# Optimization experiments

Measured on AMD Instinct MI355X. Metric: run time of the kernel, lower is better.

Reference implementation:

```python
import jax, jax.numpy as jnp
import numpy as np

B, T, H = 32, 2048, 1024

def setup_inputs() -> dict:
    key = jax.random.key(0)
    ks = jax.random.split(key, 9)
    s = 1.0 / np.sqrt(H)
    return {
        "encoder_outputs": jax.random.normal(ks[0], (B, T, H), jnp.float32),
        "decoder_output": jax.random.normal(ks[1], (1, B, H), jnp.float32),
        "Wk": jax.random.uniform(ks[2], (H, H), jnp.float32, -s, s),
        "bk": jax.random.uniform(ks[3], (H,), jnp.float32, -s, s),
        "Wq": jax.random.uniform(ks[4], (H, H), jnp.float32, -s, s),
        "bq": jax.random.uniform(ks[5], (H,), jnp.float32, -s, s),
        "Wout": jax.random.uniform(ks[6], (H,), jnp.float32, -s, s),
        "bout": jax.random.uniform(ks[7], (), jnp.float32, -s, s),
        "inputs": jax.random.randint(ks[8], (B, T), 0, 32000, jnp.int32),  # unused, as in original
    }

def reference(encoder_outputs, decoder_output, Wk, bk, Wq, bq, Wout, bout, inputs):
    # decoder_output: [1, B, H] -> [B, 1, H]
    dec = jnp.swapaxes(decoder_output, 0, 1)
    k = encoder_outputs @ Wk.T + bk          # [B, T, H]
    q = dec @ Wq.T + bq                      # [B, 1, H]
    score = jnp.tanh(k + q) @ Wout + bout    # [B, T]  (linear_out squeezed)
    attn = jax.nn.softmax(score, axis=-1)    # [B, T]
    context = jnp.einsum('bt,bth->bh', attn, encoder_outputs)  # [B, H]
    return context[:, None, :]               # [B, 1, H]
```

## Files before the change

### kernel.cpp

```cpp
#include <hip/hip_runtime.h>
#include <cmath>
#include <stdint.h>

#define B_ 32
#define T_ 2048
#define H_ 1024

typedef __attribute__((ext_vector_type(8))) __bf16 bf16x8;
typedef __attribute__((ext_vector_type(4))) float f32x4;

__device__ inline void async_copy16(const void* g, void* l) {
    __builtin_amdgcn_global_load_lds((const __attribute__((address_space(1))) uint32_t*)g,
                                     (__attribute__((address_space(3))) uint32_t*)l, 16, 0, 0);
}

__device__ inline float fast_tanh(float x) {
    float e = __expf(2.f * x);
    return 1.f - 2.f / (e + 1.f);
}

__global__ __launch_bounds__(256) void zero_kernel(float* __restrict__ p, int n) {
    int i = blockIdx.x * 256 + threadIdx.x;
    if (i < n) p[i] = 0.f;
}

__global__ __launch_bounds__(256) void convert_kernel(const float* __restrict__ in,
                                                      __bf16* __restrict__ out) {
    size_t i = (size_t)(blockIdx.x * 256 + threadIdx.x) * 8;
    const float4* p = (const float4*)(in + i);
    float4 v0 = p[0], v1 = p[1];
    bf16x8 o;
    o[0] = (__bf16)v0.x; o[1] = (__bf16)v0.y; o[2] = (__bf16)v0.z; o[3] = (__bf16)v0.w;
    o[4] = (__bf16)v1.x; o[5] = (__bf16)v1.y; o[6] = (__bf16)v1.z; o[7] = (__bf16)v1.w;
    *(bf16x8*)(out + i) = o;
}

__global__ __launch_bounds__(256) void q_kernel(const float* __restrict__ dec,
                                                const float* __restrict__ Wq,
                                                const float* __restrict__ bq,
                                                const float* __restrict__ bk,
                                                float* __restrict__ kq) {
    int b = blockIdx.x;
    int hc = blockIdx.y;
    __shared__ float ds[H_];
    for (int i = threadIdx.x; i < H_; i += 256) ds[i] = dec[b * H_ + i];
    __syncthreads();
    int h = hc * 256 + threadIdx.x;
    const float4* w = (const float4*)(Wq + (size_t)h * H_);
    float acc = 0.f;
#pragma unroll 8
    for (int j = 0; j < H_ / 4; j++) {
        float4 v = w[j];
        acc += v.x * ds[4 * j] + v.y * ds[4 * j + 1] + v.z * ds[4 * j + 2] + v.w * ds[4 * j + 3];
    }
    kq[b * H_ + h] = acc + bq[h] + bk[h];
}

__global__ __launch_bounds__(256) void score_mfma(const __bf16* __restrict__ encb,
                                                  const __bf16* __restrict__ Wkb,
                                                  const float* __restrict__ kq,
                                                  const float* __restrict__ Wout,
                                                  float* __restrict__ score) {
    __shared__ __align__(16) __bf16 As[512 * 8];
    __shared__ __align__(16) __bf16 Bs[512 * 8];

    const int h0 = blockIdx.x * 128;
    const int m0 = blockIdx.y * 128;
    const int b = m0 >> 11;
    const int tid = threadIdx.x;
    const int lane = tid & 63;
    const int w = tid >> 6;
    const int wm = w & 1, wn = w >> 1;
    const int q4 = lane >> 4, l15 = lane & 15;

    const int S0 = w * 128 + lane;
    const int S1 = S0 + 64;
    const int kg0 = S0 >> 7, row0 = S0 & 127;
    const int kg1 = S1 >> 7, row1 = S1 & 127;
    const __bf16* gA0 = encb + (size_t)(m0 + row0) * H_ + kg0 * 8;
    const __bf16* gA1 = encb + (size_t)(m0 + row1) * H_ + kg1 * 8;
    const __bf16* gB0 = Wkb + (size_t)(h0 + row0) * H_ + kg0 * 8;
    const __bf16* gB1 = Wkb + (size_t)(h0 + row1) * H_ + kg1 * 8;
    __bf16* lA0 = As + (size_t)(w * 128) * 8;
    __bf16* lA1 = As + (size_t)(w * 128 + 64) * 8;
    __bf16* lB0 = Bs + (size_t)(w * 128) * 8;
    __bf16* lB1 = Bs + (size_t)(w * 128 + 64) * 8;

    f32x4 acc[4][4];
#pragma unroll
    for (int i = 0; i < 4; i++)
#pragma unroll
        for (int j = 0; j < 4; j++) acc[i][j] = (f32x4){0.f, 0.f, 0.f, 0.f};

    for (int k0 = 0; k0 < H_; k0 += 32) {
        __syncthreads();
        async_copy16(gA0 + k0, lA0);
        async_copy16(gA1 + k0, lA1);
        async_copy16(gB0 + k0, lB0);
        async_copy16(gB1 + k0, lB1);
        __syncthreads();

        bf16x8 a[4], bb[4];
#pragma unroll
        for (int mf = 0; mf < 4; mf++)
            a[mf] = *(const bf16x8*)(As + (size_t)(q4 * 128 + wm * 64 + mf * 16 + l15) * 8);
#pragma unroll
        for (int nf = 0; nf < 4; nf++)
            bb[nf] = *(const bf16x8*)(Bs + (size_t)(q4 * 128 + wn * 64 + nf * 16 + l15) * 8);
#pragma unroll
        for (int mf = 0; mf < 4; mf++)
#pragma unroll
            for (int nf = 0; nf < 4; nf++)
                acc[mf][nf] = __builtin_amdgcn_mfma_f32_16x16x32_bf16(a[mf], bb[nf], acc[mf][nf], 0, 0, 0);
    }

    float wv[4], kqv[4];
#pragma unroll
    for (int nf = 0; nf < 4; nf++) {
        int h = h0 + wn * 64 + nf * 16 + l15;
        wv[nf] = Wout[h];
        kqv[nf] = kq[b * H_ + h];
    }
#pragma unroll
    for (int mf = 0; mf < 4; mf++) {
#pragma unroll
        for (int r = 0; r < 4; r++) {
            float s = 0.f;
#pragma unroll
            for (int nf = 0; nf < 4; nf++)
                s += wv[nf] * fast_tanh(acc[mf][nf][r] + kqv[nf]);
#pragma unroll
            for (int m = 1; m < 16; m <<= 1) s += __shfl_xor(s, m, 64);
            if (l15 == 0)
                atomicAdd(&score[m0 + wm * 64 + mf * 16 + q4 * 4 + r], s);
        }
    }
}

#define BK 32
#define ASTR 68
#define BSTR 132
__global__ __launch_bounds__(256) void score_fp32(const float* __restrict__ enc,
                                                  const float* __restrict__ Wk,
                                                  const float* __restrict__ kq,
                                                  const float* __restrict__ Wout,
                                                  float* __restrict__ score) {
    __shared__ __align__(16) float As[BK * ASTR];
    __shared__ __align__(16) float Bs[BK * BSTR];
    __shared__ float wout_s[128];
    __shared__ float kq_s[128];
    const int m0 = blockIdx.x * 64;
    const int h0 = blockIdx.y * 128;
    const int b = m0 >> 11;
    const int tid = threadIdx.x;
    const int tx = tid & 15;
    const int ty = tid >> 4;
    if (tid < 128) {
        wout_s[tid] = Wout[h0 + tid];
        kq_s[tid] = kq[b * H_ + h0 + tid];
    }
    float acc[4][8];
#pragma unroll
    for (int i = 0; i < 4; i++)
#pragma unroll
        for (int j = 0; j < 8; j++) acc[i][j] = 0.f;
    for (int k0 = 0; k0 < H_; k0 += BK) {
        __syncthreads();
#pragma unroll
        for (int r = 0; r < 2; r++) {
            int li = tid + r * 256;
            int tok = li >> 3, kg = li & 7;
            float4 v = *(const float4*)(enc + (size_t)(m0 + tok) * H_ + k0 + kg * 4);
            As[(kg * 4 + 0) * ASTR + tok] = v.x;
            As[(kg * 4 + 1) * ASTR + tok] = v.y;
            As[(kg * 4 + 2) * ASTR + tok] = v.z;
            As[(kg * 4 + 3) * ASTR + tok] = v.w;
        }
#pragma unroll
        for (int r = 0; r < 4; r++) {
            int li = tid + r * 256;
            int h = li >> 3, kg = li & 7;
            float4 v = *(const float4*)(Wk + (size_t)(h0 + h) * H_ + k0 + kg * 4);
            Bs[(kg * 4 + 0) * BSTR + h] = v.x;
            Bs[(kg * 4 + 1) * BSTR + h] = v.y;
            Bs[(kg * 4 + 2) * BSTR + h] = v.z;
            Bs[(kg * 4 + 3) * BSTR + h] = v.w;
        }
        __syncthreads();
#pragma unroll
        for (int kk = 0; kk < BK; kk++) {
            float4 a4 = *(const float4*)&As[kk * ASTR + ty * 4];
            float4 b4a = *(const float4*)&Bs[kk * BSTR + tx * 4];
            float4 b4b = *(const float4*)&Bs[kk * BSTR + 64 + tx * 4];
            float av[4] = {a4.x, a4.y, a4.z, a4.w};
            float bv[8] = {b4a.x, b4a.y, b4a.z, b4a.w, b4b.x, b4b.y, b4b.z, b4b.w};
#pragma unroll
            for (int i = 0; i < 4; i++)
#pragma unroll
                for (int j = 0; j < 8; j++) acc[i][j] += av[i] * bv[j];
        }
    }
    float wv[8], kqv[8];
#pragma unroll
    for (int j = 0; j < 8; j++) {
        int hl = (j < 4) ? (tx * 4 + j) : (64 + tx * 4 + (j - 4));
        wv[j] = wout_s[hl];
        kqv[j] = kq_s[hl];
    }
#pragma unroll
    for (int i = 0; i < 4; i++) {
        float s = 0.f;
#pragma unroll
        for (int j = 0; j < 8; j++) s += wv[j] * tanhf(acc[i][j] + kqv[j]);
#pragma unroll
        for (int m = 1; m < 16; m <<= 1) s += __shfl_xor(s, m, 64);
        if (tx == 0) atomicAdd(&score[m0 + ty * 4 + i], s);
    }
}

__global__ __launch_bounds__(256) void softmax_kernel(float* __restrict__ score) {
    int b = blockIdx.x, tid = threadIdx.x;
    float* s = score + b * T_;
    __shared__ float red[8];
    float v[8];
    float mx = -1e30f;
#pragma unroll
    for (int i = 0; i < 8; i++) {
        v[i] = s[tid + i * 256];
        mx = fmaxf(mx, v[i]);
    }
#pragma unroll
    for (int m = 32; m >= 1; m >>= 1) mx = fmaxf(mx, __shfl_xor(mx, m, 64));
    if ((tid & 63) == 0) red[tid >> 6] = mx;
    __syncthreads();
    mx = fmaxf(fmaxf(red[0], red[1]), fmaxf(red[2], red[3]));
    float sum = 0.f;
#pragma unroll
    for (int i = 0; i < 8; i++) {
        v[i] = __expf(v[i] - mx);
        sum += v[i];
    }
#pragma unroll
    for (int m = 32; m >= 1; m >>= 1) sum += __shfl_xor(sum, m, 64);
    if ((tid & 63) == 0) red[4 + (tid >> 6)] = sum;
    __syncthreads();
    sum = red[4] + red[5] + red[6] + red[7];
    float inv = 1.f / sum;
#pragma unroll
    for (int i = 0; i < 8; i++) s[tid + i * 256] = v[i] * inv;
}

__global__ __launch_bounds__(256) void context_kernel(const float* __restrict__ enc,
                                                      const float* __restrict__ attn,
                                                      float* __restrict__ out) {
    int ts = blockIdx.x, b = blockIdx.y;
    const float* e = enc + (size_t)b * T_ * H_ + (size_t)ts * 64 * H_ + threadIdx.x * 4;
    const float* a = attn + b * T_ + ts * 64;
    float4 acc = {0.f, 0.f, 0.f, 0.f};
#pragma unroll 4
    for (int t = 0; t < 64; t++) {
        float av = a[t];
        float4 v = *(const float4*)(e + (size_t)t * H_);
        acc.x += av * v.x; acc.y += av * v.y; acc.z += av * v.z; acc.w += av * v.w;
    }
    float* o = out + b * H_ + threadIdx.x * 4;
    atomicAdd(o + 0, acc.x);
    atomicAdd(o + 1, acc.y);
    atomicAdd(o + 2, acc.z);
    atomicAdd(o + 3, acc.w);
}

extern "C" void kernel_launch(void* const* d_in, const int* in_sizes, int n_in,
                              void* d_out, int out_size, void* d_ws, size_t ws_size,
                              hipStream_t stream) {
    const float* enc = (const float*)d_in[0];
    const float* dec = (const float*)d_in[1];
    const float* Wk = (const float*)d_in[2];
    const float* bk = (const float*)d_in[3];
    const float* Wq = (const float*)d_in[4];
    const float* bq = (const float*)d_in[5];
    const float* Wout = (const float*)d_in[6];
    float* out = (float*)d_out;

    const size_t encb_bytes = (size_t)B_ * T_ * H_ * 2;
    const size_t wkb_bytes = (size_t)H_ * H_ * 2;
    const size_t need = encb_bytes + wkb_bytes + (size_t)B_ * H_ * 4 + (size_t)B_ * T_ * 4;

    if (ws_size >= need) {
        __bf16* encb = (__bf16*)d_ws;
        __bf16* Wkb = (__bf16*)((char*)d_ws + encb_bytes);
        float* kq = (float*)((char*)d_ws + encb_bytes + wkb_bytes);
        float* score = kq + B_ * H_;

        convert_kernel<<<(B_ * T_ * H_) / 2048, 256, 0, stream>>>(enc, encb);
        convert_kernel<<<(H_ * H_) / 2048, 256, 0, stream>>>(Wk, Wkb);
        q_kernel<<<dim3(B_, 4), 256, 0, stream>>>(dec, Wq, bq, bk, kq);
        zero_kernel<<<(B_ * T_ + 255) / 256, 256, 0, stream>>>(score, B_ * T_);
        zero_kernel<<<(B_ * H_ + 255) / 256, 256, 0, stream>>>(out, B_ * H_);
        score_mfma<<<dim3(8, 512), 256, 0, stream>>>(encb, Wkb, kq, Wout, score);
        softmax_kernel<<<B_, 256, 0, stream>>>(score);
        context_kernel<<<dim3(32, B_), 256, 0, stream>>>(enc, score, out);
    } else {
        float* kq = (float*)d_ws;
        float* score = kq + B_ * H_;
        q_kernel<<<dim3(B_, 4), 256, 0, stream>>>(dec, Wq, bq, bk, kq);
        zero_kernel<<<(B_ * T_ + 255) / 256, 256, 0, stream>>>(score, B_ * T_);
        zero_kernel<<<(B_ * H_ + 255) / 256, 256, 0, stream>>>(out, B_ * H_);
        score_fp32<<<dim3(1024, 8), 256, 0, stream>>>(enc, Wk, kq, Wout, score);
        softmax_kernel<<<B_, 256, 0, stream>>>(score);
        context_kernel<<<dim3(32, B_), 256, 0, stream>>>(enc, score, out);
    }
}
```

Before: 761.2 us.

## Deepen MFMA K-tile, remap blocks per XCD, replace atomics with partial-sum buffers

The score GEMM now stages a 64-wide K slice per iteration instead of 32, halving barrier and loop overhead. It also uses a 1D grid whose block index is remapped so that M-tiles sharing the same XCD reuse L2. Atomic score accumulation is replaced by 16 per-column-slice partial buffers that the softmax kernel sums. The context atomics are likewise replaced by per-chunk partials plus a separate reduce kernel, which drops the zero kernels. The cost is more workspace, extra global traffic for the partials, one more launch, and larger shared memory per block that may lower occupancy.

```diff
diff --git a/kernel.cpp b/kernel.cpp
--- a/kernel.cpp
+++ b/kernel.cpp
@@ -60,12 +60,16 @@
                                                   const __bf16* __restrict__ Wkb,
                                                   const float* __restrict__ kq,
                                                   const float* __restrict__ Wout,
-                                                  float* __restrict__ score) {
-    __shared__ __align__(16) __bf16 As[512 * 8];
-    __shared__ __align__(16) __bf16 Bs[512 * 8];
-
-    const int h0 = blockIdx.x * 128;
-    const int m0 = blockIdx.y * 128;
+                                                  float* __restrict__ sp) {
+    __shared__ __align__(16) __bf16 As[1024 * 8];
+    __shared__ __align__(16) __bf16 Bs[1024 * 8];
+
+    const int bid = blockIdx.x;
+    const int xcd = bid & 7;
+    const int g = (bid >> 3) & 7;
+    const int mt = (bid >> 6) * 8 + xcd;
+    const int h0 = g * 128;
+    const int m0 = mt * 128;
     const int b = m0 >> 11;
     const int tid = threadIdx.x;
     const int lane = tid & 63;
@@ -73,18 +77,19 @@
     const int wm = w & 1, wn = w >> 1;
     const int q4 = lane >> 4, l15 = lane & 15;
 
-    const int S0 = w * 128 + lane;
-    const int S1 = S0 + 64;
-    const int kg0 = S0 >> 7, row0 = S0 & 127;
-    const int kg1 = S1 >> 7, row1 = S1 & 127;
-    const __bf16* gA0 = encb + (size_t)(m0 + row0) * H_ + kg0 * 8;
-    const __bf16* gA1 = encb + (size_t)(m0 + row1) * H_ + kg1 * 8;
-    const __bf16* gB0 = Wkb + (size_t)(h0 + row0) * H_ + kg0 * 8;
-    const __bf16* gB1 = Wkb + (size_t)(h0 + row1) * H_ + kg1 * 8;
-    __bf16* lA0 = As + (size_t)(w * 128) * 8;
-    __bf16* lA1 = As + (size_t)(w * 128 + 64) * 8;
-    __bf16* lB0 = Bs + (size_t)(w * 128) * 8;
-    __bf16* lB1 = Bs + (size_t)(w * 128 + 64) * 8;
+    int kgs[4], rows[4];
+    const __bf16 *gA[4], *gB[4];
+    __bf16 *lA[4], *lB[4];
+#pragma unroll
+    for (int r = 0; r < 4; r++) {
+        int S = w * 256 + r * 64 + lane;
+        kgs[r] = S >> 7;
+        rows[r] = S & 127;
+        gA[r] = encb + (size_t)(m0 + rows[r]) * H_ + kgs[r] * 8;
+        gB[r] = Wkb + (size_t)(h0 + rows[r]) * H_ + kgs[r] * 8;
+        lA[r] = As + (size_t)(w * 256 + r * 64) * 8;
+        lB[r] = Bs + (size_t)(w * 256 + r * 64) * 8;
+    }
 
     f32x4 acc[4][4];
 #pragma unroll
@@ -92,26 +97,29 @@
 #pragma unroll
         for (int j = 0; j < 4; j++) acc[i][j] = (f32x4){0.f, 0.f, 0.f, 0.f};
 
-    for (int k0 = 0; k0 < H_; k0 += 32) {
+    for (int k0 = 0; k0 < H_; k0 += 64) {
         __syncthreads();
-        async_copy16(gA0 + k0, lA0);
-        async_copy16(gA1 + k0, lA1);
-        async_copy16(gB0 + k0, lB0);
-        async_copy16(gB1 + k0, lB1);
+#pragma unroll
+        for (int r = 0; r < 4; r++) async_copy16(gA[r] + k0, lA[r]);
+#pragma unroll
+        for (int r = 0; r < 4; r++) async_copy16(gB[r] + k0, lB[r]);
         __syncthreads();
 
-        bf16x8 a[4], bb[4];
-#pragma unroll
-        for (int mf = 0; mf < 4; mf++)
-            a[mf] = *(const bf16x8*)(As + (size_t)(q4 * 128 + wm * 64 + mf * 16 + l15) * 8);
-#pragma unroll
-        for (int nf = 0; nf < 4; nf++)
-            bb[nf] = *(const bf16x8*)(Bs + (size_t)(q4 * 128 + wn * 64 + nf * 16 + l15) * 8);
-#pragma unroll
-        for (int mf = 0; mf < 4; mf++)
+#pragma unroll
+        for (int kb = 0; kb < 2; kb++) {
+            bf16x8 a[4], bb[4];
+#pragma unroll
+            for (int mf = 0; mf < 4; mf++)
+                a[mf] = *(const bf16x8*)(As + (size_t)(((kb * 4 + q4) * 128) + wm * 64 + mf * 16 + l15) * 8);
 #pragma unroll
             for (int nf = 0; nf < 4; nf++)
-                acc[mf][nf] = __builtin_amdgcn_mfma_f32_16x16x32_bf16(a[mf], bb[nf], acc[mf][nf], 0, 0, 0);
+                bb[nf] = *(const bf16x8*)(Bs + (size_t)(((kb * 4 + q4) * 128) + wn * 64 + nf * 16 + l15) * 8);
+#pragma unroll
+            for (int mf = 0; mf < 4; mf++)
+#pragma unroll
+                for (int nf = 0; nf < 4; nf++)
+                    acc[mf][nf] = __builtin_amdgcn_mfma_f32_16x16x32_bf16(a[mf], bb[nf], acc[mf][nf], 0, 0, 0);
+        }
     }
 
     float wv[4], kqv[4];
@@ -121,6 +129,7 @@
         wv[nf] = Wout[h];
         kqv[nf] = kq[b * H_ + h];
     }
+    const size_t slice = (size_t)(g * 2 + wn) * (B_ * T_);
 #pragma unroll
     for (int mf = 0; mf < 4; mf++) {
 #pragma unroll
@@ -132,9 +141,71 @@
 #pragma unroll
             for (int m = 1; m < 16; m <<= 1) s += __shfl_xor(s, m, 64);
             if (l15 == 0)
-                atomicAdd(&score[m0 + wm * 64 + mf * 16 + q4 * 4 + r], s);
-        }
-    }
+                sp[slice + m0 + wm * 64 + mf * 16 + q4 * 4 + r] = s;
+        }
+    }
+}
+
+__global__ __launch_bounds__(256) void softmax_kernel(const float* __restrict__ sp,
+                                                      float* __restrict__ attn) {
+    int b = blockIdx.x, tid = threadIdx.x;
+    __shared__ float red[8];
+    float v[8];
+    float mx = -1e30f;
+#pragma unroll
+    for (int i = 0; i < 8; i++) {
+        int t = tid + i * 256;
+        float s = 0.f;
+#pragma unroll
+        for (int sl = 0; sl < 16; sl++) s += sp[(size_t)sl * (B_ * T_) + b * T_ + t];
+        v[i] = s;
+        mx = fmaxf(mx, s);
+    }
+#pragma unroll
+    for (int m = 32; m >= 1; m >>= 1) mx = fmaxf(mx, __shfl_xor(mx, m, 64));
+    if ((tid & 63) == 0) red[tid >> 6] = mx;
+    __syncthreads();
+    mx = fmaxf(fmaxf(red[0], red[1]), fmaxf(red[2], red[3]));
+    float sum = 0.f;
+#pragma unroll
+    for (int i = 0; i < 8; i++) {
+        v[i] = __expf(v[i] - mx);
+        sum += v[i];
+    }
+#pragma unroll
+    for (int m = 32; m >= 1; m >>= 1) sum += __shfl_xor(sum, m, 64);
+    if ((tid & 63) == 0) red[4 + (tid >> 6)] = sum;
+    __syncthreads();
+    sum = red[4] + red[5] + red[6] + red[7];
+    float inv = 1.f / sum;
+#pragma unroll
+    for (int i = 0; i < 8; i++) attn[b * T_ + tid + i * 256] = v[i] * inv;
+}
+
+__global__ __launch_bounds__(256) void context_part(const float* __restrict__ enc,
+                                                    const float* __restrict__ attn,
+                                                    float* __restrict__ cpart) {
+    int ts = blockIdx.x, b = blockIdx.y;
+    const float* e = enc + (size_t)b * T_ * H_ + (size_t)ts * 64 * H_ + threadIdx.x * 4;
+    const float* a = attn + b * T_ + ts * 64;
+    float4 acc = {0.f, 0.f, 0.f, 0.f};
+#pragma unroll 4
+    for (int t = 0; t < 64; t++) {
+        float av = a[t];
+        float4 v = *(const float4*)(e + (size_t)t * H_);
+        acc.x += av * v.x; acc.y += av * v.y; acc.z += av * v.z; acc.w += av * v.w;
+    }
+    *(float4*)(cpart + ((size_t)b * 32 + ts) * H_ + threadIdx.x * 4) = acc;
+}
+
+__global__ __launch_bounds__(256) void context_reduce(const float* __restrict__ cpart,
+                                                      float* __restrict__ out) {
+    int hc = blockIdx.x, b = blockIdx.y;
+    int h = hc * 256 + threadIdx.x;
+    float s = 0.f;
+#pragma unroll
+    for (int ts = 0; ts < 32; ts++) s += cpart[((size_t)b * 32 + ts) * H_ + h];
+    out[b * H_ + h] = s;
 }
 
 #define BK 32
@@ -145,8 +216,8 @@
                                                   const float* __restrict__ kq,
                                                   const float* __restrict__ Wout,
                                                   float* __restrict__ score) {
-    __shared__ __align__(16) float As[BK * ASTR];
-    __shared__ __align__(16) float Bs[BK * BSTR];
+    __shared__ __align__(16) float As2[BK * ASTR];
+    __shared__ __align__(16) float Bs2[BK * BSTR];
     __shared__ float wout_s[128];
     __shared__ float kq_s[128];
     const int m0 = blockIdx.x * 64;
@@ -171,27 +242,27 @@
             int li = tid + r * 256;
             int tok = li >> 3, kg = li & 7;
             float4 v = *(const float4*)(enc + (size_t)(m0 + tok) * H_ + k0 + kg * 4);
-            As[(kg * 4 + 0) * ASTR + tok] = v.x;
-            As[(kg * 4 + 1) * ASTR + tok] = v.y;
-            As[(kg * 4 + 2) * ASTR + tok] = v.z;
-            As[(kg * 4 + 3) * ASTR + tok] = v.w;
+            As2[(kg * 4 + 0) * ASTR + tok] = v.x;
+            As2[(kg * 4 + 1) * ASTR + tok] = v.y;
+            As2[(kg * 4 + 2) * ASTR + tok] = v.z;
+            As2[(kg * 4 + 3) * ASTR + tok] = v.w;
         }
 #pragma unroll
         for (int r = 0; r < 4; r++) {
             int li = tid + r * 256;
             int h = li >> 3, kg = li & 7;
             float4 v = *(const float4*)(Wk + (size_t)(h0 + h) * H_ + k0 + kg * 4);
-            Bs[(kg * 4 + 0) * BSTR + h] = v.x;
-            Bs[(kg * 4 + 1) * BSTR + h] = v.y;
-            Bs[(kg * 4 + 2) * BSTR + h] = v.z;
-            Bs[(kg * 4 + 3) * BSTR + h] = v.w;
+            Bs2[(kg * 4 + 0) * BSTR + h] = v.x;
+            Bs2[(kg * 4 + 1) * BSTR + h] = v.y;
+            Bs2[(kg * 4 + 2) * BSTR + h] = v.z;
+            Bs2[(kg * 4 + 3) * BSTR + h] = v.w;
         }
         __syncthreads();
 #pragma unroll
         for (int kk = 0; kk < BK; kk++) {
-            float4 a4 = *(const float4*)&As[kk * ASTR + ty * 4];
-            float4 b4a = *(const float4*)&Bs[kk * BSTR + tx * 4];
-            float4 b4b = *(const float4*)&Bs[kk * BSTR + 64 + tx * 4];
+            float4 a4 = *(const float4*)&As2[kk * ASTR + ty * 4];
+            float4 b4a = *(const float4*)&Bs2[kk * BSTR + tx * 4];
+            float4 b4b = *(const float4*)&Bs2[kk * BSTR + 64 + tx * 4];
             float av[4] = {a4.x, a4.y, a4.z, a4.w};
             float bv[8] = {b4a.x, b4a.y, b4a.z, b4a.w, b4b.x, b4b.y, b4b.z, b4b.w};
 #pragma unroll
@@ -218,7 +289,7 @@
     }
 }
 
-__global__ __launch_bounds__(256) void softmax_kernel(float* __restrict__ score) {
+__global__ __launch_bounds__(256) void softmax_inplace(float* __restrict__ score) {
     int b = blockIdx.x, tid = threadIdx.x;
     float* s = score + b * T_;
     __shared__ float red[8];
@@ -248,26 +319,6 @@
     float inv = 1.f / sum;
 #pragma unroll
     for (int i = 0; i < 8; i++) s[tid + i * 256] = v[i] * inv;
-}
-
-__global__ __launch_bounds__(256) void context_kernel(const float* __restrict__ enc,
-                                                      const float* __restrict__ attn,
-                                                      float* __restrict__ out) {
-    int ts = blockIdx.x, b = blockIdx.y;
-    const float* e = enc + (size_t)b * T_ * H_ + (size_t)ts * 64 * H_ + threadIdx.x * 4;
-    const float* a = attn + b * T_ + ts * 64;
-    float4 acc = {0.f, 0.f, 0.f, 0.f};
-#pragma unroll 4
-    for (int t = 0; t < 64; t++) {
-        float av = a[t];
-        float4 v = *(const float4*)(e + (size_t)t * H_);
-        acc.x += av * v.x; acc.y += av * v.y; acc.z += av * v.z; acc.w += av * v.w;
-    }
-    float* o = out + b * H_ + threadIdx.x * 4;
-    atomicAdd(o + 0, acc.x);
-    atomicAdd(o + 1, acc.y);
-    atomicAdd(o + 2, acc.z);
-    atomicAdd(o + 3, acc.w);
 }
 
 extern "C" void kernel_launch(void* const* d_in, const int* in_sizes, int n_in,
@@ -284,30 +335,38 @@
 
     const size_t encb_bytes = (size_t)B_ * T_ * H_ * 2;
     const size_t wkb_bytes = (size_t)H_ * H_ * 2;
-    const size_t need = encb_bytes + wkb_bytes + (size_t)B_ * H_ * 4 + (size_t)B_ * T_ * 4;
+    const size_t kq_bytes = (size_t)B_ * H_ * 4;
+    const size_t attn_bytes = (size_t)B_ * T_ * 4;
+    const size_t sp_bytes = (size_t)16 * B_ * T_ * 4;
+    const size_t cpart_bytes = (size_t)B_ * 32 * H_ * 4;
+    const size_t shared_bytes = sp_bytes > cpart_bytes ? sp_bytes : cpart_bytes;
+    const size_t need = encb_bytes + wkb_bytes + kq_bytes + attn_bytes + shared_bytes;
 
     if (ws_size >= need) {
-        __bf16* encb = (__bf16*)d_ws;
-        __bf16* Wkb = (__bf16*)((char*)d_ws + encb_bytes);
-        float* kq = (float*)((char*)d_ws + encb_bytes + wkb_bytes);
-        float* score = kq + B_ * H_;
+        char* p = (char*)d_ws;
+        __bf16* encb = (__bf16*)p;            p += encb_bytes;
+        __bf16* Wkb = (__bf16*)p;             p += wkb_bytes;
+        float* kq = (float*)p;                p += kq_bytes;
+        float* attn = (float*)p;              p += attn_bytes;
+        float* sp = (float*)p;
+        float* cpart = (float*)p;
 
         convert_kernel<<<(B_ * T_ * H_) / 2048, 256, 0, stream>>>(enc, encb);
         convert_kernel<<<(H_ * H_) / 2048, 256, 0, stream>>>(Wk, Wkb);
         q_kernel<<<dim3(B_, 4), 256, 0, stream>>>(dec, Wq, bq, bk, kq);
-        zero_kernel<<<(B_ * T_ + 255) / 256, 256, 0, stream>>>(score, B_ * T_);
-        zero_kernel<<<(B_ * H_ + 255) / 256, 256, 0, stream>>>(out, B_ * H_);
-        score_mfma<<<dim3(8, 512), 256, 0, stream>>>(encb, Wkb, kq, Wout, score);
-        softmax_kernel<<<B_, 256, 0, stream>>>(score);
-        context_kernel<<<dim3(32, B_), 256, 0, stream>>>(enc, score, out);
+        score_mfma<<<4096, 256, 0, stream>>>(encb, Wkb, kq, Wout, sp);
+        softmax_kernel<<<B_, 256, 0, stream>>>(sp, attn);
+        context_part<<<dim3(32, B_), 256, 0, stream>>>(enc, attn, cpart);
+        context_reduce<<<dim3(4, B_), 256, 0, stream>>>(cpart, out);
     } else {
         float* kq = (float*)d_ws;
         float* score = kq + B_ * H_;
+        float* cpart = score + B_ * T_;
         q_kernel<<<dim3(B_, 4), 256, 0, stream>>>(dec, Wq, bq, bk, kq);
         zero_kernel<<<(B_ * T_ + 255) / 256, 256, 0, stream>>>(score, B_ * T_);
-        zero_kernel<<<(B_ * H_ + 255) / 256, 256, 0, stream>>>(out, B_ * H_);
         score_fp32<<<dim3(1024, 8), 256, 0, stream>>>(enc, Wk, kq, Wout, score);
-        softmax_kernel<<<B_, 256, 0, stream>>>(score);
-        context_kernel<<<dim3(32, B_), 256, 0, stream>>>(enc, score, out);
-    }
-}
+        softmax_inplace<<<B_, 256, 0, stream>>>(score);
+        context_part<<<dim3(32, B_), 256, 0, stream>>>(enc, score, cpart);
+        context_reduce<<<dim3(4, B_), 256, 0, stream>>>(cpart, out);
+    }
+}
```

Result: no change. 772.6 us (+1.5%).
